# Performance work log

Measured on AMD Instinct MI355X. Metric: run time of the kernel, lower is better.

Reference implementation:

```python
import jax, jax.numpy as jnp
import numpy as np

B, N_ATOM, N_TOK, ATOMS_PER_TOK = 4, 1024, 256, 4
BOND_PROB = 0.02


def setup_inputs() -> dict:
    key = jax.random.key(0)
    k1, k2 = jax.random.split(key)
    atom_pad_mask = jnp.ones((B, N_ATOM), dtype=bool)
    atom_mono_idx = jax.random.randint(k1, (B, N_ATOM), 0, 4) - 1
    # symmetric sparse token-token bond matrix, trailing singleton dim like the torch feats
    u = jax.random.uniform(k2, (B, N_TOK, N_TOK))
    sym = (u + jnp.swapaxes(u, 1, 2)) * 0.5
    token_bonds = (sym < BOND_PROB).astype(jnp.float32)[..., None]
    # one-hot atom -> token map, ATOMS_PER_TOK consecutive atoms per token
    tok_idx = jnp.arange(N_ATOM) // ATOMS_PER_TOK
    atom_to_token = jnp.broadcast_to(
        jax.nn.one_hot(tok_idx, N_TOK, dtype=jnp.float32), (B, N_ATOM, N_TOK)
    )
    return {
        "atom_pad_mask": atom_pad_mask,
        "atom_mono_idx": atom_mono_idx,
        "token_bonds": token_bonds,
        "atom_to_token": atom_to_token,
    }


def _floyd_warshall(dist):
    # dist: (B, N, N) float, inf = unreachable. Sequential min-plus rank-1 updates.
    Bb, N, _ = dist.shape

    def body(d, k):
        col = jax.lax.dynamic_slice(d, (0, 0, k), (Bb, N, 1))  # d[:, :, k]
        row = jax.lax.dynamic_slice(d, (0, k, 0), (Bb, 1, N))  # d[:, k, :]
        return jnp.minimum(d, col + row), None

    dist, _ = jax.lax.scan(body, dist, jnp.arange(N))
    return dist


def reference(atom_pad_mask, atom_mono_idx, token_bonds, atom_to_token):
    Bb, N = atom_pad_mask.shape
    tb = token_bonds[..., 0] > 0                      # (B, T, T) bool
    idx = jnp.argmax(atom_to_token, axis=-1)          # (B, N) atom -> token
    # atom-level adjacency: adj[b,i,j] = tb[b, idx[b,i], idx[b,j]]
    adj = jax.vmap(lambda t, i: t[i][:, i])(tb, idx)  # (B, N, N) bool
    g = atom_mono_idx != -1                           # glycan-atom mask (B, N)
    pair = g[:, :, None] & g[:, None, :]              # glycan-glycan pairs
    eye = jnp.eye(N, dtype=bool)[None]
    # init: 1 for bonded glycan pairs, 0 on glycan diagonal, inf elsewhere.
    # Non-glycan atoms stay at inf everywhere (incl. diagonal) so paths never
    # route through them -- equivalent to FW on the compact glycan subgraph.
    dist0 = jnp.where(adj & pair, 1.0, jnp.inf)
    dist0 = jnp.where(eye & g[:, :, None], 0.0, dist0)
    dist = _floyd_warshall(dist0)
    # scatter back: -1 (infinite_dist) for non-glycan pairs / unreachable,
    # then diagonal forced to 0 for every atom (as in the torch code).
    out = jnp.where(pair & jnp.isfinite(dist), dist, -1.0)
    out = jnp.where(eye, 0.0, out)
    return out.astype(jnp.int32)
```

## Files before the change

kernel.cpp:

```cpp
#include <hip/hip_runtime.h>
#include <stdint.h>

#define BATCH 4
#define NATOM 1024
#define NTOK  256

typedef unsigned short u16x8 __attribute__((ext_vector_type(8)));
typedef unsigned long long u64;

#define OFF_ADJ  0
#define OFF_DIST 32768
#define OFF_TOK  557056
#define OFF_G    573440
#define OFF_L    577536

__global__ __launch_bounds__(256) void k_prep(const int* __restrict__ mono,
                                              const float* __restrict__ a2t,
                                              const float* __restrict__ bonds,
                                              int* __restrict__ tok,
                                              unsigned char* __restrict__ g,
                                              u64* __restrict__ adjw) {
    int bid  = blockIdx.x;
    int wave = threadIdx.x >> 6;
    int lane = threadIdx.x & 63;
    if (bid < 1024) {
        int atom = bid * 4 + wave;
        const float* row = a2t + (size_t)atom * NTOK + lane * 4;
        float4 v = *(const float4*)row;
        float mv = v.x; int mi = lane * 4;
        if (v.y > mv) { mv = v.y; mi = lane * 4 + 1; }
        if (v.z > mv) { mv = v.z; mi = lane * 4 + 2; }
        if (v.w > mv) { mv = v.w; mi = lane * 4 + 3; }
        #pragma unroll
        for (int off = 32; off > 0; off >>= 1) {
            float ov = __shfl_down(mv, off);
            int   oi = __shfl_down(mi, off);
            if (ov > mv || (ov == mv && oi < mi)) { mv = ov; mi = oi; }
        }
        if (lane == 0) {
            tok[atom] = mi;
            g[atom]   = (mono[atom] != -1) ? 1 : 0;
        }
    } else {
        int row = (bid - 1024) * 4 + wave;
        const float* p = bonds + (size_t)row * NTOK;
        u64 w0 = __ballot(p[lane]       > 0.0f);
        u64 w1 = __ballot(p[lane + 64]  > 0.0f);
        u64 w2 = __ballot(p[lane + 128] > 0.0f);
        u64 w3 = __ballot(p[lane + 192] > 0.0f);
        if (lane == 0) {
            u64* d = adjw + (size_t)row * 4;
            d[0] = w0; d[1] = w1; d[2] = w2; d[3] = w3;
        }
    }
}

__global__ __launch_bounds__(256) void k_bfs(const int* __restrict__ tok,
                                             const unsigned char* __restrict__ g,
                                             const u64* __restrict__ adjw,
                                             unsigned short* __restrict__ distws,
                                             unsigned short* __restrict__ Lws) {
    int b = blockIdx.x;
    int t = threadIdx.x;
    extern __shared__ char smem[];
    unsigned short* dist = (unsigned short*)smem;
    u64* adjm            = (u64*)(smem + 131072);
    unsigned* usable32   = (unsigned*)(smem + 131072 + 8192);

    if (t < 8) usable32[t] = 0;
    {
        u16x8 ff = {0xFFFF,0xFFFF,0xFFFF,0xFFFF,0xFFFF,0xFFFF,0xFFFF,0xFFFF};
        u16x8* dp = (u16x8*)dist;
        #pragma unroll
        for (int k = 0; k < 32; ++k) dp[t + k * 256] = ff;
    }
    __syncthreads();
    #pragma unroll
    for (int q = 0; q < 4; ++q) {
        int a = b * NATOM + t + q * 256;
        if (g[a]) {
            int tt = tok[a];
            atomicOr(&usable32[tt >> 5], 1u << (tt & 31));
        }
    }
    __syncthreads();
    u64 um0 = ((u64)usable32[1] << 32) | usable32[0];
    u64 um1 = ((u64)usable32[3] << 32) | usable32[2];
    u64 um2 = ((u64)usable32[5] << 32) | usable32[4];
    u64 um3 = ((u64)usable32[7] << 32) | usable32[6];
    {
        const u64* arow = adjw + (size_t)(b * NTOK + t) * 4;
        u64 a0 = arow[0], a1 = arow[1], a2 = arow[2], a3 = arow[3];
        int w = t >> 6;
        u64 bt = 1ull << (t & 63);
        bool ut = (((w == 0) ? um0 : (w == 1) ? um1 : (w == 2) ? um2 : um3) >> (t & 63)) & 1;
        u64 m0 = ut ? (a0 & um0) : 0ull;
        u64 m1 = ut ? (a1 & um1) : 0ull;
        u64 m2 = ut ? (a2 & um2) : 0ull;
        u64 m3 = ut ? (a3 & um3) : 0ull;
        adjm[t * 4 + 0] = m0; adjm[t * 4 + 1] = m1;
        adjm[t * 4 + 2] = m2; adjm[t * 4 + 3] = m3;
        u64 selfbit = (((w == 0) ? a0 : (w == 1) ? a1 : (w == 2) ? a2 : a3) >> (t & 63)) & 1;
        u64 e0 = m0, e1 = m1, e2 = m2, e3 = m3;
        if (w == 0) e0 &= ~bt; else if (w == 1) e1 &= ~bt;
        else if (w == 2) e2 &= ~bt; else e3 &= ~bt;
        bool nb = (e0 | e1 | e2 | e3) != 0ull;
        Lws[b * NTOK + t] = selfbit ? 1 : (nb ? 2 : 0x7FFF);
    }
    __syncthreads();
    {
        int w = t >> 6;
        u64 bt = 1ull << (t & 63);
        u64 r0 = (w == 0) ? bt : 0ull, r1 = (w == 1) ? bt : 0ull;
        u64 r2 = (w == 2) ? bt : 0ull, r3 = (w == 3) ? bt : 0ull;
        u64 f0 = r0, f1 = r1, f2 = r2, f3 = r3;
        unsigned short* drow = dist + t * 256;
        for (int level = 1; level < 256; ++level) {
            u64 nx0 = 0, nx1 = 0, nx2 = 0, nx3 = 0;
#define EXPAND_WORD(F, W) { u64 f_ = (F); while (f_) { int v_ = ((W) << 6) + __builtin_ctzll(f_); f_ &= f_ - 1; \
            nx0 |= adjm[v_ * 4 + 0]; nx1 |= adjm[v_ * 4 + 1]; nx2 |= adjm[v_ * 4 + 2]; nx3 |= adjm[v_ * 4 + 3]; } }
            EXPAND_WORD(f0, 0) EXPAND_WORD(f1, 1) EXPAND_WORD(f2, 2) EXPAND_WORD(f3, 3)
#undef EXPAND_WORD
            u64 n0 = nx0 & ~r0, n1 = nx1 & ~r1, n2 = nx2 & ~r2, n3 = nx3 & ~r3;
            if (!(n0 | n1 | n2 | n3)) break;
#define RECORD_WORD(NW, W) { u64 n_ = (NW); while (n_) { int v_ = ((W) << 6) + __builtin_ctzll(n_); n_ &= n_ - 1; \
            drow[v_] = (unsigned short)level; } }
            RECORD_WORD(n0, 0) RECORD_WORD(n1, 1) RECORD_WORD(n2, 2) RECORD_WORD(n3, 3)
#undef RECORD_WORD
            r0 |= n0; r1 |= n1; r2 |= n2; r3 |= n3;
            f0 = n0; f1 = n1; f2 = n2; f3 = n3;
        }
    }
    __syncthreads();
    {
        const u16x8* src = (const u16x8*)dist;
        u16x8* dst = (u16x8*)(distws + (size_t)b * NTOK * NTOK);
        #pragma unroll
        for (int k = 0; k < 32; ++k) dst[t + k * 256] = src[t + k * 256];
    }
}

__global__ __launch_bounds__(256) void k_expand(const int* __restrict__ tok,
                                                const unsigned char* __restrict__ g,
                                                const unsigned short* __restrict__ D,
                                                const unsigned short* __restrict__ L,
                                                int* __restrict__ out) {
    int b = blockIdx.x >> 10;
    int i = blockIdx.x & 1023;
    int t4 = threadIdx.x;
    int base = b * NATOM;
    int ti = tok[base + i];
    int gi = g[base + i];
    const unsigned short* Drow = D + ((size_t)b * NTOK + ti) * NTOK;
    int Li = L[b * NTOK + ti];
    int Lval = (Li <= 255) ? Li : -1;
    int4 tj4 = ((const int4*)(tok + base))[t4];
    uchar4 g4 = ((const uchar4*)(g + base))[t4];
    int j0 = t4 * 4;
    int4 o;
    {
        int j = j0, tj = tj4.x, gj = g4.x;
        o.x = (i == j) ? 0 : ((!gi || !gj) ? -1 : ((tj == ti) ? Lval
              : ((Drow[tj] <= 255) ? (int)Drow[tj] : -1)));
    }
    {
        int j = j0 + 1, tj = tj4.y, gj = g4.y;
        o.y = (i == j) ? 0 : ((!gi || !gj) ? -1 : ((tj == ti) ? Lval
              : ((Drow[tj] <= 255) ? (int)Drow[tj] : -1)));
    }
    {
        int j = j0 + 2, tj = tj4.z, gj = g4.z;
        o.z = (i == j) ? 0 : ((!gi || !gj) ? -1 : ((tj == ti) ? Lval
              : ((Drow[tj] <= 255) ? (int)Drow[tj] : -1)));
    }
    {
        int j = j0 + 3, tj = tj4.w, gj = g4.w;
        o.w = (i == j) ? 0 : ((!gi || !gj) ? -1 : ((tj == ti) ? Lval
              : ((Drow[tj] <= 255) ? (int)Drow[tj] : -1)));
    }
    ((int4*)(out + ((size_t)(base + i)) * NATOM))[t4] = o;
}

extern "C" void kernel_launch(void* const* d_in, const int* in_sizes, int n_in,
                              void* d_out, int out_size, void* d_ws, size_t ws_size,
                              hipStream_t stream) {
    const int*   mono  = (const int*)d_in[1];
    const float* bonds = (const float*)d_in[2];
    const float* a2t   = (const float*)d_in[3];

    char* ws = (char*)d_ws;
    u64* adjw           = (u64*)(ws + OFF_ADJ);
    unsigned short* dist = (unsigned short*)(ws + OFF_DIST);
    int* tok            = (int*)(ws + OFF_TOK);
    unsigned char* g    = (unsigned char*)(ws + OFF_G);
    unsigned short* L   = (unsigned short*)(ws + OFF_L);

    k_prep<<<1280, 256, 0, stream>>>(mono, a2t, bonds, tok, g, adjw);
    k_bfs<<<BATCH, 256, 139296, stream>>>(tok, g, adjw, dist, L);
    k_expand<<<BATCH * NATOM, 256, 0, stream>>>(tok, g, dist, L, (int*)d_out);
}
```

Before: 82.45 us.

## Split token BFS across 16 blocks with 4 lanes cooperating per source

The all-pairs BFS kernel now launches 16 blocks (4 per batch, 64 source tokens each) instead of 4 blocks, and each source is handled by 4 lanes that each own one 64-bit frontier word and combine neighbor masks with xor-shuffles. This spreads the serial BFS over more CUs and splits per-source frontier expansion four ways. Shared memory per block shrinks to a 64-row distance tile, traded against redundant adjacency setup in every block and extra shuffle reductions per level.

```diff
diff --git a/kernel.cpp b/kernel.cpp
--- a/kernel.cpp
+++ b/kernel.cpp
@@ -60,19 +60,19 @@
                                              const u64* __restrict__ adjw,
                                              unsigned short* __restrict__ distws,
                                              unsigned short* __restrict__ Lws) {
-    int b = blockIdx.x;
-    int t = threadIdx.x;
-    extern __shared__ char smem[];
-    unsigned short* dist = (unsigned short*)smem;
-    u64* adjm            = (u64*)(smem + 131072);
-    unsigned* usable32   = (unsigned*)(smem + 131072 + 8192);
+    int b     = blockIdx.x >> 2;
+    int chunk = blockIdx.x & 3;
+    int t     = threadIdx.x;
+    __shared__ u64 adjm[NTOK * 4];
+    __shared__ unsigned usable32[8];
+    __shared__ unsigned short dist[64 * NTOK];
 
     if (t < 8) usable32[t] = 0;
     {
         u16x8 ff = {0xFFFF,0xFFFF,0xFFFF,0xFFFF,0xFFFF,0xFFFF,0xFFFF,0xFFFF};
         u16x8* dp = (u16x8*)dist;
         #pragma unroll
-        for (int k = 0; k < 32; ++k) dp[t + k * 256] = ff;
+        for (int k = 0; k < 8; ++k) dp[t + k * 256] = ff;
     }
     __syncthreads();
     #pragma unroll
@@ -100,43 +100,60 @@
         u64 m3 = ut ? (a3 & um3) : 0ull;
         adjm[t * 4 + 0] = m0; adjm[t * 4 + 1] = m1;
         adjm[t * 4 + 2] = m2; adjm[t * 4 + 3] = m3;
-        u64 selfbit = (((w == 0) ? a0 : (w == 1) ? a1 : (w == 2) ? a2 : a3) >> (t & 63)) & 1;
-        u64 e0 = m0, e1 = m1, e2 = m2, e3 = m3;
-        if (w == 0) e0 &= ~bt; else if (w == 1) e1 &= ~bt;
-        else if (w == 2) e2 &= ~bt; else e3 &= ~bt;
-        bool nb = (e0 | e1 | e2 | e3) != 0ull;
-        Lws[b * NTOK + t] = selfbit ? 1 : (nb ? 2 : 0x7FFF);
-    }
-    __syncthreads();
-    {
-        int w = t >> 6;
-        u64 bt = 1ull << (t & 63);
-        u64 r0 = (w == 0) ? bt : 0ull, r1 = (w == 1) ? bt : 0ull;
-        u64 r2 = (w == 2) ? bt : 0ull, r3 = (w == 3) ? bt : 0ull;
-        u64 f0 = r0, f1 = r1, f2 = r2, f3 = r3;
-        unsigned short* drow = dist + t * 256;
+        if (chunk == 0) {
+            u64 selfbit = (((w == 0) ? a0 : (w == 1) ? a1 : (w == 2) ? a2 : a3) >> (t & 63)) & 1;
+            u64 e0 = m0, e1 = m1, e2 = m2, e3 = m3;
+            if (w == 0) e0 &= ~bt; else if (w == 1) e1 &= ~bt;
+            else if (w == 2) e2 &= ~bt; else e3 &= ~bt;
+            bool nb = (e0 | e1 | e2 | e3) != 0ull;
+            Lws[b * NTOK + t] = selfbit ? 1 : (nb ? 2 : 0x7FFF);
+        }
+    }
+    __syncthreads();
+    {
+        int sl = t >> 2;
+        int w  = t & 3;
+        int s  = chunk * 64 + sl;
+        u64 r = ((s >> 6) == w) ? (1ull << (s & 63)) : 0ull;
+        u64 f = r;
+        unsigned short* drow = dist + sl * 256;
+        const ulonglong2* adj2 = (const ulonglong2*)adjm;
         for (int level = 1; level < 256; ++level) {
-            u64 nx0 = 0, nx1 = 0, nx2 = 0, nx3 = 0;
-#define EXPAND_WORD(F, W) { u64 f_ = (F); while (f_) { int v_ = ((W) << 6) + __builtin_ctzll(f_); f_ &= f_ - 1; \
-            nx0 |= adjm[v_ * 4 + 0]; nx1 |= adjm[v_ * 4 + 1]; nx2 |= adjm[v_ * 4 + 2]; nx3 |= adjm[v_ * 4 + 3]; } }
-            EXPAND_WORD(f0, 0) EXPAND_WORD(f1, 1) EXPAND_WORD(f2, 2) EXPAND_WORD(f3, 3)
-#undef EXPAND_WORD
-            u64 n0 = nx0 & ~r0, n1 = nx1 & ~r1, n2 = nx2 & ~r2, n3 = nx3 & ~r3;
-            if (!(n0 | n1 | n2 | n3)) break;
-#define RECORD_WORD(NW, W) { u64 n_ = (NW); while (n_) { int v_ = ((W) << 6) + __builtin_ctzll(n_); n_ &= n_ - 1; \
-            drow[v_] = (unsigned short)level; } }
-            RECORD_WORD(n0, 0) RECORD_WORD(n1, 1) RECORD_WORD(n2, 2) RECORD_WORD(n3, 3)
-#undef RECORD_WORD
-            r0 |= n0; r1 |= n1; r2 |= n2; r3 |= n3;
-            f0 = n0; f1 = n1; f2 = n2; f3 = n3;
+            u64 p0 = 0, p1 = 0, p2 = 0, p3 = 0;
+            u64 f_ = f;
+            while (f_) {
+                int v = (w << 6) + __builtin_ctzll(f_);
+                f_ &= f_ - 1;
+                ulonglong2 q01 = adj2[v * 2];
+                ulonglong2 q23 = adj2[v * 2 + 1];
+                p0 |= q01.x; p1 |= q01.y; p2 |= q23.x; p3 |= q23.y;
+            }
+            p0 |= __shfl_xor(p0, 1); p0 |= __shfl_xor(p0, 2);
+            p1 |= __shfl_xor(p1, 1); p1 |= __shfl_xor(p1, 2);
+            p2 |= __shfl_xor(p2, 1); p2 |= __shfl_xor(p2, 2);
+            p3 |= __shfl_xor(p3, 1); p3 |= __shfl_xor(p3, 2);
+            u64 full = (w == 0) ? p0 : (w == 1) ? p1 : (w == 2) ? p2 : p3;
+            u64 nw = full & ~r;
+            int flag = (nw != 0ull);
+            flag |= __shfl_xor(flag, 1);
+            flag |= __shfl_xor(flag, 2);
+            if (!flag) break;
+            u64 n_ = nw;
+            while (n_) {
+                int v = (w << 6) + __builtin_ctzll(n_);
+                n_ &= n_ - 1;
+                drow[v] = (unsigned short)level;
+            }
+            r |= nw;
+            f = nw;
         }
     }
     __syncthreads();
     {
         const u16x8* src = (const u16x8*)dist;
-        u16x8* dst = (u16x8*)(distws + (size_t)b * NTOK * NTOK);
+        u16x8* dst = (u16x8*)(distws + ((size_t)b * NTOK + chunk * 64) * NTOK);
         #pragma unroll
-        for (int k = 0; k < 32; ++k) dst[t + k * 256] = src[t + k * 256];
+        for (int k = 0; k < 8; ++k) dst[t + k * 256] = src[t + k * 256];
     }
 }
 
@@ -189,13 +206,13 @@
     const float* a2t   = (const float*)d_in[3];
 
     char* ws = (char*)d_ws;
-    u64* adjw           = (u64*)(ws + OFF_ADJ);
+    u64* adjw            = (u64*)(ws + OFF_ADJ);
     unsigned short* dist = (unsigned short*)(ws + OFF_DIST);
-    int* tok            = (int*)(ws + OFF_TOK);
-    unsigned char* g    = (unsigned char*)(ws + OFF_G);
-    unsigned short* L   = (unsigned short*)(ws + OFF_L);
+    int* tok             = (int*)(ws + OFF_TOK);
+    unsigned char* g     = (unsigned char*)(ws + OFF_G);
+    unsigned short* L    = (unsigned short*)(ws + OFF_L);
 
     k_prep<<<1280, 256, 0, stream>>>(mono, a2t, bonds, tok, g, adjw);
-    k_bfs<<<BATCH, 256, 139296, stream>>>(tok, g, adjw, dist, L);
+    k_bfs<<<16, 256, 0, stream>>>(tok, g, adjw, dist, L);
     k_expand<<<BATCH * NATOM, 256, 0, stream>>>(tok, g, dist, L, (int*)d_out);
 }
```

New measurement: 81.33 us. No clear change (-1.4%).
